# Performance work log

Measured on AMD Instinct MI355X. Metric: run time of the kernel, lower is better.

Reference implementation:

```python
import jax, jax.numpy as jnp
import numpy as np
from jax import lax

B, T, F, H, NSTEPS = 512, 512, 64, 128, 8
HALF = H // 2
LN_EPS = 1e-5


def gru_cell(x, h, w_ih, w_hh, b_ih, b_hh):
    # PyTorch GRUCell math. x: (B, in), h: (B, H)
    gx = x @ w_ih.T + b_ih            # (B, 3H)
    gh = h @ w_hh.T + b_hh            # (B, 3H)
    rx, zx, nx = jnp.split(gx, 3, axis=-1)
    rh, zh, nh = jnp.split(gh, 3, axis=-1)
    r = jax.nn.sigmoid(rx + rh)
    z = jax.nn.sigmoid(zx + zh)
    n = jnp.tanh(nx + r * nh)
    return (1.0 - z) * n + z * h


def run_gru_layer(xs, h0, w_ih, w_hh, b_ih, b_hh):
    # xs: (T, B, in) -> (T, B, H), last hidden (B, H)
    def step(h, x_t):
        h = gru_cell(x_t, h, w_ih, w_hh, b_ih, b_hh)
        return h, h
    h_last, ys = lax.scan(step, h0, xs)
    return ys, h_last


def setup_inputs() -> dict:
    key = jax.random.key(0)
    ks = iter(jax.random.split(key, 64))
    s = 1.0 / np.sqrt(H)

    def p(shape):
        return jax.random.uniform(next(ks), shape, jnp.float32, -s, s)

    inp = {"x": jax.random.normal(next(ks), (B, T, F), jnp.float32)}
    # encoder: 3 GRU layers (layer 0 takes F features, layers 1-2 take H)
    for l, d_in in enumerate([F, H, H]):
        inp[f"e{l}w_ih"] = p((3 * H, d_in))
        inp[f"e{l}w_hh"] = p((3 * H, H))
        inp[f"e{l}b_ih"] = p((3 * H,))
        inp[f"e{l}b_hh"] = p((3 * H,))
    # additive (Bahdanau) attention
    inp["aWq"] = p((H, H)); inp["abq"] = p((H,))
    inp["aWk"] = p((H, H)); inp["abk"] = p((H,))
    inp["av"] = p((H,))
    # decoder GRU: input is cat([context, state]) -> 2H
    inp["dw_ih"] = p((3 * H, 2 * H)); inp["dw_hh"] = p((3 * H, H))
    inp["db_ih"] = p((3 * H,)); inp["db_hh"] = p((3 * H,))
    # head: LayerNorm -> Linear(H, H/2) -> ReLU -> Linear(H/2, 1)
    inp["lng"] = jnp.ones((H,), jnp.float32); inp["lnb"] = jnp.zeros((H,), jnp.float32)
    inp["w1"] = p((HALF, H)); inp["b1"] = p((HALF,))
    inp["w2"] = p((1, HALF)); inp["b2"] = p((1,))
    return inp


def reference(x,
              e0w_ih, e0w_hh, e0b_ih, e0b_hh,
              e1w_ih, e1w_hh, e1b_ih, e1b_hh,
              e2w_ih, e2w_hh, e2b_ih, e2b_hh,
              aWq, abq, aWk, abk, av,
              dw_ih, dw_hh, db_ih, db_hh,
              lng, lnb, w1, b1, w2, b2):
    b = x.shape[0]
    xs = jnp.transpose(x, (1, 0, 2))  # (T, B, F)
    h0 = jnp.zeros((b, H), x.dtype)
    # 3-layer encoder GRU (dropout is eval-mode no-op)
    ys, _ = run_gru_layer(xs, h0, e0w_ih, e0w_hh, e0b_ih, e0b_hh)
    ys, _ = run_gru_layer(ys, h0, e1w_ih, e1w_hh, e1b_ih, e1b_hh)
    ys, h_n = run_gru_layer(ys, h0, e2w_ih, e2w_hh, e2b_ih, e2b_hh)
    enc = jnp.transpose(ys, (1, 0, 2))  # (B, T, H)

    keys = enc @ aWk.T + abk  # precompute key projection once: (B, T, H)

    def dec_step(h, _):
        q = h @ aWq.T + abq                                   # (B, H)
        scores = jnp.einsum('bth,h->bt', jnp.tanh(keys + q[:, None, :]), av)
        w = jax.nn.softmax(scores, axis=-1)                   # (B, T)
        ctx = jnp.einsum('bt,bth->bh', w, enc)                # (B, H)
        h_new = gru_cell(jnp.concatenate([ctx, h], axis=-1), h,
                         dw_ih, dw_hh, db_ih, db_hh)
        mu = h_new.mean(-1, keepdims=True)
        var = ((h_new - mu) ** 2).mean(-1, keepdims=True)
        y = (h_new - mu) / jnp.sqrt(var + LN_EPS) * lng + lnb
        y = jax.nn.relu(y @ w1.T + b1)
        pred = y @ w2.T + b2                                  # (B, 1)
        return h_new, pred

    _, preds = lax.scan(dec_step, h_n, None, length=NSTEPS)   # (n_steps, B, 1)
    return jnp.transpose(preds, (1, 0, 2))                    # (B, n_steps, 1)
```

## Files before the change

kernel.cpp:

```cpp
#include <hip/hip_runtime.h>
#include <hip/hip_bf16.h>
#include <cstdint>
#include <cstddef>

#define T_LEN 512
#define B_SZ  512
#define F_IN  64
#define H_DIM 128
#define NSTEP 8

typedef __attribute__((ext_vector_type(8))) short short8;
typedef __attribute__((ext_vector_type(4))) float f32x4;

__device__ __forceinline__ float fsig(float x) { return 1.0f / (1.0f + __expf(-x)); }
__device__ __forceinline__ float ftanh(float x) {
  float e = __expf(-2.0f * fabsf(x));
  float t = (1.0f - e) / (1.0f + e);
  return copysignf(t, x);
}
__device__ __forceinline__ unsigned short bf16hi(float x) {
  __hip_bfloat16 h = __float2bfloat16(x);
  return *(unsigned short*)&h;
}
__device__ __forceinline__ float bf2f(unsigned short u) {
  return __uint_as_float(((unsigned)u) << 16);
}
__device__ __forceinline__ float bflo(unsigned u) { return __uint_as_float(u << 16); }
__device__ __forceinline__ float bfhi(unsigned u) { return __uint_as_float(u & 0xffff0000u); }

template <int CTRL>
__device__ __forceinline__ float dpp_add(float v) {
  int p = __builtin_amdgcn_update_dpp(0, __float_as_int(v), CTRL, 0xF, 0xF, true);
  return v + __int_as_float(p);
}
__device__ __forceinline__ float row_sum16(float v) {
  v = dpp_add<0xB1>(v);
  v = dpp_add<0x4E>(v);
  v = dpp_add<0x124>(v);
  v = dpp_add<0x128>(v);
  return v;
}

__device__ __forceinline__ void split8(const float* p, short8& hi, short8& lo) {
  #pragma unroll
  for (int i = 0; i < 8; ++i) {
    const float v = p[i];
    const unsigned short h = bf16hi(v);
    hi[i] = (short)h;
    lo[i] = (short)bf16hi(v - bf2f(h));
  }
}

__device__ __forceinline__ void split_f4pair(const float4 a, const float4 b,
                                             short8& hi, short8& lo) {
  const float v[8] = {a.x, a.y, a.z, a.w, b.x, b.y, b.z, b.w};
  #pragma unroll
  for (int j = 0; j < 8; ++j) {
    const unsigned short h = bf16hi(v[j]);
    hi[j] = (short)h;
    lo[j] = (short)bf16hi(v[j] - bf2f(h));
  }
}

__global__ __launch_bounds__(256) void prep_split(
    const float* __restrict__ w0, const float* __restrict__ w1,
    const float* __restrict__ w2,
    unsigned short* __restrict__ hi, unsigned short* __restrict__ lo)
{
  const int i = blockIdx.x * 256 + threadIdx.x;
  if (i >= 122880) return;
  float v = (i < 24576) ? w0[i] : ((i < 73728) ? w1[i - 24576] : w2[i - 73728]);
  const unsigned short h = bf16hi(v);
  hi[i] = h;
  lo[i] = bf16hi(v - bf2f(h));
}

template <int IS_L0>
__global__ __launch_bounds__(512, 2) void rec_fused(
    const float* x,
    const unsigned short* Xhi,
    const unsigned short* Xlo,
    const unsigned short* __restrict__ Wih_hi,
    const unsigned short* __restrict__ Wih_lo,
    const float* __restrict__ w_hh, const float* __restrict__ b_ih,
    const float* __restrict__ b_hh,
    unsigned short* Hhi, unsigned short* Hlo)
{
  constexpr int KD   = IS_L0 ? 64 : 128;
  constexpr int NCK  = KD / 32;
  constexpr int WROW = KD * 2;
  constexpr int WGRAN = WROW / 16;
  constexpr int XBUF = IS_L0 ? 4096 : 8192;

  __shared__ unsigned short Wlds[384 * KD];
  __shared__ float gxlds[8 * 2 * 384];
  __shared__ unsigned short hbh[2][2048], hbl[2][2048];
  __shared__ unsigned short hsh[2][256], hsl[2][256];
  __shared__ __align__(16) unsigned char Xraw[2][XBUF];

  const int tid  = threadIdx.x;
  const int wv   = tid >> 6, lane = tid & 63;
  const int quad = lane >> 4, l16 = lane & 15;
  const int b0   = blockIdx.x * 2;
  const int c    = wv * 16 + l16;

  {
    unsigned char* wb = (unsigned char*)Wlds;
    #pragma unroll
    for (int k = 0; k < (384 * WGRAN) / 512; ++k) {
      const int idx = k * 512 + tid;
      const int row = idx / WGRAN;
      const int gg  = idx % WGRAN;
      const uint4 v = *(const uint4*)&Wih_hi[(size_t)row * KD + gg * 8];
      *(uint4*)&wb[row * WROW + ((gg ^ (row & 7)) * 16)] = v;
    }
  }

  short8 Wl_[3][NCK];
  #pragma unroll
  for (int g_ = 0; g_ < 3; ++g_)
    #pragma unroll
    for (int ck = 0; ck < NCK; ++ck)
      Wl_[g_][ck] = *(const short8*)&Wih_lo[(size_t)(g_ * 128 + c) * KD + ck * 32 + quad * 8];

  short8 Bh[3][4], Bl[3][4];
  #pragma unroll
  for (int g_ = 0; g_ < 3; ++g_)
    #pragma unroll
    for (int ck = 0; ck < 4; ++ck)
      split8(&w_hh[(size_t)(g_ * 128 + c) * 128 + ck * 32 + quad * 8],
             Bh[g_][ck], Bl[g_][ck]);

  float bias_r = 0.f, bias_z = 0.f, bihn = 0.f, bhhn = 0.f, h0 = 0.f, h1 = 0.f;
  if (quad == 0) {
    bias_r = b_ih[c] + b_hh[c];
    bias_z = b_ih[c + 128] + b_hh[c + 128];
    bihn = b_ih[c + 256];
    bhhn = b_hh[c + 256];
    hsh[0][c] = 0; hsh[0][128 + c] = 0;
    hsl[0][c] = 0; hsl[0][128 + c] = 0;
  }

  const int t8 = tid & 255;
  const int sr = t8 >> 4;
  const int sg = tid & 15;
  uint4 xr = {0, 0, 0, 0};

  auto load_xr = [&](int tgn) {
    if constexpr (IS_L0) {
      if (tid < 256)
        xr = *(const uint4*)&x[((size_t)(b0 + (sr & 1)) * T_LEN + tgn + (sr >> 1)) * 64 + sg * 4];
    } else {
      const unsigned short* src = (tid < 256) ? Xhi : Xlo;
      xr = *(const uint4*)&src[((size_t)(tgn + (sr >> 1)) * B_SZ + b0 + (sr & 1)) * 128 + sg * 8];
    }
  };
  auto store_xr = [&](int buf) {
    unsigned char* dstb = &Xraw[buf][0];
    const int off = sr * 256 + ((sg ^ (sr & 7)) * 16);
    if constexpr (IS_L0) {
      if (tid < 256) *(uint4*)&dstb[off] = xr;
    } else {
      *(uint4*)&dstb[(tid < 256 ? 0 : 4096) + off] = xr;
    }
  };
  auto flush_h = [&](int buf, int tp) {
    const int ft = t8 >> 5, fr = (t8 >> 4) & 1, fs = t8 & 15;
    const size_t go = ((size_t)(tp + ft) * B_SZ + b0 + fr) * 128 + fs * 8;
    const int lo_ = (ft * 2 + fr) * 128 + fs * 8;
    if (tid < 256) *(uint4*)&Hhi[go] = *(const uint4*)&hbh[buf][lo_];
    else           *(uint4*)&Hlo[go] = *(const uint4*)&hbl[buf][lo_];
  };

  load_xr(0);
  store_xr(0);
  load_xr(8);
  __syncthreads();

  for (int g = 0; g < 64; ++g) {
    if (g > 0) flush_h((g - 1) & 1, g * 8 - 8);

    short8 Xhf[NCK], Xlf[NCK];
    {
      const unsigned char* xbuf = &Xraw[g & 1][0];
      if constexpr (IS_L0) {
        #pragma unroll
        for (int ck = 0; ck < 2; ++ck) {
          const int g0 = ck * 8 + quad * 2;
          const float4 f0 = *(const float4*)&xbuf[l16 * 256 + ((g0 ^ (l16 & 7)) * 16)];
          const float4 f1 = *(const float4*)&xbuf[l16 * 256 + (((g0 + 1) ^ (l16 & 7)) * 16)];
          split_f4pair(f0, f1, Xhf[ck], Xlf[ck]);
        }
      } else {
        #pragma unroll
        for (int ck = 0; ck < 4; ++ck) {
          const int go = ((ck * 4 + quad) ^ (l16 & 7)) * 16;
          Xhf[ck] = *(const short8*)&xbuf[l16 * 256 + go];
          Xlf[ck] = *(const short8*)&xbuf[4096 + l16 * 256 + go];
        }
      }
    }
    {
      f32x4 ax[3][2];
      #pragma unroll
      for (int g_ = 0; g_ < 3; ++g_) {
        ax[g_][0] = (f32x4){0.f, 0.f, 0.f, 0.f};
        ax[g_][1] = (f32x4){0.f, 0.f, 0.f, 0.f};
      }
      const unsigned char* wb = (const unsigned char*)Wlds;
      #pragma unroll
      for (int ck = 0; ck < NCK; ++ck) {
        const int p = (NCK == 4) ? (ck >> 1) : ck;
        #pragma unroll
        for (int g_ = 0; g_ < 3; ++g_) {
          const int n = g_ * 128 + c;
          const short8 wh = *(const short8*)&wb[n * WROW + (((ck * 4 + quad) ^ (n & 7)) * 16)];
          ax[g_][p] = __builtin_amdgcn_mfma_f32_16x16x32_bf16(Xhf[ck], wh, ax[g_][p], 0, 0, 0);
          ax[g_][p] = __builtin_amdgcn_mfma_f32_16x16x32_bf16(Xhf[ck], Wl_[g_][ck], ax[g_][p], 0, 0, 0);
          ax[g_][p] = __builtin_amdgcn_mfma_f32_16x16x32_bf16(Xlf[ck], wh, ax[g_][p], 0, 0, 0);
        }
      }
      #pragma unroll
      for (int g_ = 0; g_ < 3; ++g_)
        #pragma unroll
        for (int reg = 0; reg < 4; ++reg) {
          const int tt_ = quad * 2 + (reg >> 1);
          const int r_  = reg & 1;
          gxlds[(tt_ * 2 + r_) * 384 + g_ * 128 + c] = ax[g_][0][reg] + ax[g_][1][reg];
        }
    }
    __syncthreads();

    #pragma unroll
    for (int tt = 0; tt < 8; ++tt) {
      float gr0 = 0.f, gz0 = 0.f, gn0 = 0.f, gr1 = 0.f, gz1 = 0.f, gn1 = 0.f;
      if (quad == 0) {
        const float* gp = &gxlds[tt * 768 + c];
        gr0 = gp[0];   gz0 = gp[128]; gn0 = gp[256];
        gr1 = gp[384]; gz1 = gp[512]; gn1 = gp[640];
      }

      short8 Ahf[4], Alf[4];
      if (l16 < 2) {
        #pragma unroll
        for (int ck = 0; ck < 4; ++ck) {
          const int ad = l16 * 128 + ck * 32 + quad * 8;
          Ahf[ck] = *(const short8*)&hsh[tt & 1][ad];
          Alf[ck] = *(const short8*)&hsl[tt & 1][ad];
        }
      } else {
        #pragma unroll
        for (int ck = 0; ck < 4; ++ck) {
          Ahf[ck] = (short8){0, 0, 0, 0, 0, 0, 0, 0};
          Alf[ck] = (short8){0, 0, 0, 0, 0, 0, 0, 0};
        }
      }

      f32x4 acc[3][2];
      #pragma unroll
      for (int g_ = 0; g_ < 3; ++g_) {
        acc[g_][0] = (f32x4){0.f, 0.f, 0.f, 0.f};
        acc[g_][1] = (f32x4){0.f, 0.f, 0.f, 0.f};
      }
      #pragma unroll
      for (int ck = 0; ck < 4; ++ck) {
        const int p = ck >> 1;
        #pragma unroll
        for (int g_ = 0; g_ < 3; ++g_) {
          acc[g_][p] = __builtin_amdgcn_mfma_f32_16x16x32_bf16(Ahf[ck], Bh[g_][ck], acc[g_][p], 0, 0, 0);
          acc[g_][p] = __builtin_amdgcn_mfma_f32_16x16x32_bf16(Ahf[ck], Bl[g_][ck], acc[g_][p], 0, 0, 0);
          acc[g_][p] = __builtin_amdgcn_mfma_f32_16x16x32_bf16(Alf[ck], Bh[g_][ck], acc[g_][p], 0, 0, 0);
        }
      }

      if (quad == 0) {
        const float ghr0 = acc[0][0][0] + acc[0][1][0];
        const float ghr1 = acc[0][0][1] + acc[0][1][1];
        const float ghz0 = acc[1][0][0] + acc[1][1][0];
        const float ghz1 = acc[1][0][1] + acc[1][1][1];
        const float ghn0 = acc[2][0][0] + acc[2][1][0];
        const float ghn1 = acc[2][0][1] + acc[2][1][1];
        const float r0 = fsig(gr0 + ghr0 + bias_r);
        const float z0 = fsig(gz0 + ghz0 + bias_z);
        const float nv0 = ftanh(gn0 + bihn + r0 * (ghn0 + bhhn));
        const float hn0 = (1.0f - z0) * nv0 + z0 * h0;
        const float r1 = fsig(gr1 + ghr1 + bias_r);
        const float z1 = fsig(gz1 + ghz1 + bias_z);
        const float nv1 = ftanh(gn1 + bihn + r1 * (ghn1 + bhhn));
        const float hn1 = (1.0f - z1) * nv1 + z1 * h1;
        h0 = hn0; h1 = hn1;
        const int nb = (tt + 1) & 1;
        const unsigned short hh0 = bf16hi(hn0), hh1 = bf16hi(hn1);
        const unsigned short hl0 = bf16hi(hn0 - bf2f(hh0));
        const unsigned short hl1 = bf16hi(hn1 - bf2f(hh1));
        hsh[nb][c] = hh0;       hsh[nb][128 + c] = hh1;
        hsl[nb][c] = hl0;       hsl[nb][128 + c] = hl1;
        const int hb = (tt * 2) * 128 + c;
        hbh[g & 1][hb] = hh0;       hbh[g & 1][hb + 128] = hh1;
        hbl[g & 1][hb] = hl0;       hbl[g & 1][hb + 128] = hl1;
      }

      if (tt == 7 && g + 1 < 64) {
        store_xr((g + 1) & 1);
        if (g + 2 < 64) load_xr((g + 2) * 8);
      }
      __syncthreads();
    }
  }
  flush_h(1, 504);
}

__global__ __launch_bounds__(256) void keys_gemm(
    const unsigned short* __restrict__ Ahi, const unsigned short* __restrict__ Alo,
    const float* __restrict__ aWk, const float* __restrict__ abk,
    unsigned short* __restrict__ Khi)
{
  __shared__ unsigned short Ah[64 * 40], Al[64 * 40];
  __shared__ unsigned short Bh[128 * 136], Bl[128 * 136];
  const int tid  = threadIdx.x;
  const int wave = tid >> 6, lane = tid & 63;
  const int quad = lane >> 4, l16 = lane & 15;
  const size_t m0 = (size_t)blockIdx.x * 64;

  for (int i = tid; i < 16384; i += 256) {
    const float v = aWk[i];
    const unsigned short h = bf16hi(v);
    const int r = i >> 7, k = i & 127;
    Bh[r * 136 + k] = h;
    Bl[r * 136 + k] = bf16hi(v - bf2f(h));
  }

  f32x4 acc[8];
  #pragma unroll
  for (int i = 0; i < 8; ++i) acc[i] = (f32x4){0.f, 0.f, 0.f, 0.f};
  float bias[8];
  #pragma unroll
  for (int nt = 0; nt < 8; ++nt) bias[nt] = abk[nt * 16 + l16];

  const int r = tid >> 2, c8 = (tid & 3) * 8;
  for (int kc = 0; kc < 128; kc += 32) {
    __syncthreads();
    const size_t src = (m0 + r) * 128 + kc + c8;
    *(uint4*)&Ah[r * 40 + c8] = *(const uint4*)&Ahi[src];
    *(uint4*)&Al[r * 40 + c8] = *(const uint4*)&Alo[src];
    __syncthreads();
    const short8 a_hi = *(const short8*)&Ah[(wave * 16 + l16) * 40 + quad * 8];
    const short8 a_lo = *(const short8*)&Al[(wave * 16 + l16) * 40 + quad * 8];
    #pragma unroll
    for (int nt = 0; nt < 8; ++nt) {
      const short8 b_hi = *(const short8*)&Bh[(nt * 16 + l16) * 136 + kc + quad * 8];
      const short8 b_lo = *(const short8*)&Bl[(nt * 16 + l16) * 136 + kc + quad * 8];
      acc[nt] = __builtin_amdgcn_mfma_f32_16x16x32_bf16(a_hi, b_hi, acc[nt], 0, 0, 0);
      acc[nt] = __builtin_amdgcn_mfma_f32_16x16x32_bf16(a_hi, b_lo, acc[nt], 0, 0, 0);
      acc[nt] = __builtin_amdgcn_mfma_f32_16x16x32_bf16(a_lo, b_hi, acc[nt], 0, 0, 0);
    }
  }
  #pragma unroll
  for (int nt = 0; nt < 8; ++nt) {
    #pragma unroll
    for (int reg = 0; reg < 4; ++reg) {
      const size_t m = m0 + wave * 16 + quad * 4 + reg;
      const int n = nt * 16 + l16;
      Khi[m * 128 + n] = bf16hi(acc[nt][reg] + bias[nt]);
    }
  }
}

__global__ __launch_bounds__(512) void decoder(
    const unsigned short* __restrict__ Hhi, const unsigned short* __restrict__ Hlo,
    const unsigned short* __restrict__ Khi,
    const float* __restrict__ aWq, const float* __restrict__ abq,
    const float* __restrict__ av,
    const float* __restrict__ dwih, const float* __restrict__ dwhh,
    const float* __restrict__ dbih, const float* __restrict__ dbhh,
    const float* __restrict__ lng, const float* __restrict__ lnb,
    const float* __restrict__ w1, const float* __restrict__ b1,
    const float* __restrict__ w2, const float* __restrict__ b2,
    float* __restrict__ out)
{
  __shared__ float h_s[128], q_s[128], av_s[128], s_s[512], w_s[512];
  __shared__ float part[8][128], u_s[256], gx_s[384], gh_s[384], y_s[128];
  __shared__ float red[16];
  const int b = blockIdx.x, tid = threadIdx.x;
  const int wave = tid >> 6, lane = tid & 63;
  const int tslot = lane >> 4, ks = lane & 15;

  if (tid < 128) {
    const size_t base = ((size_t)(T_LEN - 1) * B_SZ + b) * 128 + tid;
    h_s[tid] = bf2f(Hhi[base]) + bf2f(Hlo[base]);
    av_s[tid] = av[tid];
  }
  __syncthreads();

  for (int step = 0; step < NSTEP; ++step) {
    if (tid < 128) {
      float acc = abq[tid];
      const float* wr = &aWq[(size_t)tid * 128];
      #pragma unroll 8
      for (int k4 = 0; k4 < 32; ++k4) {
        const float4 hv = *(const float4*)&h_s[k4 * 4];
        const float4 wv = *(const float4*)&wr[k4 * 4];
        acc += hv.x * wv.x + hv.y * wv.y + hv.z * wv.z + hv.w * wv.w;
      }
      q_s[tid] = acc;
    }
    __syncthreads();
    #pragma unroll 2
    for (int it = 0; it < 16; ++it) {
      const int t = it * 32 + wave * 4 + tslot;
      const size_t kb = ((size_t)t * B_SZ + b) * 128 + ks * 8;
      const uint4 uh = *(const uint4*)&Khi[kb];
      const float4 q0 = *(const float4*)&q_s[ks * 8];
      const float4 q1 = *(const float4*)&q_s[ks * 8 + 4];
      const float4 a0 = *(const float4*)&av_s[ks * 8];
      const float4 a1 = *(const float4*)&av_s[ks * 8 + 4];
      float acc = ftanh(bflo(uh.x) + q0.x) * a0.x + ftanh(bfhi(uh.x) + q0.y) * a0.y
                + ftanh(bflo(uh.y) + q0.z) * a0.z + ftanh(bfhi(uh.y) + q0.w) * a0.w
                + ftanh(bflo(uh.z) + q1.x) * a1.x + ftanh(bfhi(uh.z) + q1.y) * a1.y
                + ftanh(bflo(uh.w) + q1.z) * a1.z + ftanh(bfhi(uh.w) + q1.w) * a1.w;
      acc = row_sum16(acc);
      if (ks == 0) s_s[t] = acc;
    }
    __syncthreads();
    {
      const float sv = s_s[tid];
      float mx = sv;
      #pragma unroll
      for (int o = 32; o; o >>= 1) mx = fmaxf(mx, __shfl_xor(mx, o, 64));
      if (lane == 0) red[wave] = mx;
      __syncthreads();
      mx = red[0];
      #pragma unroll
      for (int i = 1; i < 8; ++i) mx = fmaxf(mx, red[i]);
      const float e = __expf(sv - mx);
      float sm = e;
      #pragma unroll
      for (int o = 32; o; o >>= 1) sm += __shfl_xor(sm, o, 64);
      if (lane == 0) red[8 + wave] = sm;
      __syncthreads();
      float tot = red[8];
      #pragma unroll
      for (int i = 1; i < 8; ++i) tot += red[8 + i];
      w_s[tid] = e / tot;
    }
    __syncthreads();
    {
      const int th = tid >> 6;
      const int c2 = (tid & 63) * 2;
      float acc0 = 0.0f, acc1 = 0.0f;
      #pragma unroll 4
      for (int q = 0; q < 64; ++q) {
        const int t = th * 64 + q;
        const unsigned u = *(const unsigned*)&Hhi[((size_t)t * B_SZ + b) * 128 + c2];
        const float wt = w_s[t];
        acc0 += wt * bflo(u);
        acc1 += wt * bfhi(u);
      }
      part[th][c2] = acc0;
      part[th][c2 + 1] = acc1;
    }
    __syncthreads();
    if (tid < 128) {
      float s = part[0][tid];
      #pragma unroll
      for (int i = 1; i < 8; ++i) s += part[i][tid];
      u_s[tid] = s;
      u_s[128 + tid] = h_s[tid];
    }
    __syncthreads();
    if (tid < 384) {
      const int j = tid;
      float gxv = dbih[j], ghv = dbhh[j];
      const float* wxr = &dwih[(size_t)j * 256];
      const float* whr = &dwhh[(size_t)j * 128];
      #pragma unroll 8
      for (int k4 = 0; k4 < 64; ++k4) {
        const float4 uv = *(const float4*)&u_s[k4 * 4];
        const float4 wv = *(const float4*)&wxr[k4 * 4];
        gxv += uv.x * wv.x + uv.y * wv.y + uv.z * wv.z + uv.w * wv.w;
      }
      #pragma unroll 8
      for (int k4 = 0; k4 < 32; ++k4) {
        const float4 hv = *(const float4*)&h_s[k4 * 4];
        const float4 wv = *(const float4*)&whr[k4 * 4];
        ghv += hv.x * wv.x + hv.y * wv.y + hv.z * wv.z + hv.w * wv.w;
      }
      gx_s[j] = gxv; gh_s[j] = ghv;
    }
    __syncthreads();
    if (tid < 128) {
      const float r = fsig(gx_s[tid] + gh_s[tid]);
      const float z = fsig(gx_s[128 + tid] + gh_s[128 + tid]);
      const float n = ftanh(gx_s[256 + tid] + r * gh_s[256 + tid]);
      const float hn = (1.0f - z) * n + z * h_s[tid];
      h_s[tid] = hn;
      float s1 = hn, s2 = hn * hn;
      #pragma unroll
      for (int o = 32; o; o >>= 1) { s1 += __shfl_xor(s1, o, 64); s2 += __shfl_xor(s2, o, 64); }
      if ((tid & 63) == 0) { red[tid >> 6] = s1; red[4 + (tid >> 6)] = s2; }
    }
    __syncthreads();
    if (tid < 128) {
      const float hn  = h_s[tid];
      const float mu  = (red[0] + red[1]) * (1.0f / 128.0f);
      const float var = (red[4] + red[5]) * (1.0f / 128.0f) - mu * mu;
      y_s[tid] = (hn - mu) / sqrtf(var + 1e-5f) * lng[tid] + lnb[tid];
    }
    __syncthreads();
    if (tid < 64) {
      float acc = b1[tid];
      const float* wr = &w1[(size_t)tid * 128];
      #pragma unroll 8
      for (int k4 = 0; k4 < 32; ++k4) {
        const float4 yv = *(const float4*)&y_s[k4 * 4];
        const float4 wv = *(const float4*)&wr[k4 * 4];
        acc += yv.x * wv.x + yv.y * wv.y + yv.z * wv.z + yv.w * wv.w;
      }
      acc = fmaxf(acc, 0.0f);
      float v = acc * w2[tid];
      #pragma unroll
      for (int o = 32; o; o >>= 1) v += __shfl_xor(v, o, 64);
      if (tid == 0) out[(size_t)b * NSTEP + step] = v + b2[0];
    }
    __syncthreads();
  }
}

extern "C" void kernel_launch(void* const* d_in, const int* in_sizes, int n_in,
                              void* d_out, int out_size, void* d_ws, size_t ws_size,
                              hipStream_t stream)
{
  (void)in_sizes; (void)n_in; (void)out_size; (void)ws_size;
  const float* x    = (const float*)d_in[0];
  const float* ewih[3] = {(const float*)d_in[1], (const float*)d_in[5], (const float*)d_in[9]};
  const float* ewhh[3] = {(const float*)d_in[2], (const float*)d_in[6], (const float*)d_in[10]};
  const float* ebih[3] = {(const float*)d_in[3], (const float*)d_in[7], (const float*)d_in[11]};
  const float* ebhh[3] = {(const float*)d_in[4], (const float*)d_in[8], (const float*)d_in[12]};
  const float* aWq  = (const float*)d_in[13];
  const float* abq  = (const float*)d_in[14];
  const float* aWk  = (const float*)d_in[15];
  const float* abk  = (const float*)d_in[16];
  const float* av   = (const float*)d_in[17];
  const float* dwih = (const float*)d_in[18];
  const float* dwhh = (const float*)d_in[19];
  const float* dbih = (const float*)d_in[20];
  const float* dbhh = (const float*)d_in[21];
  const float* lng  = (const float*)d_in[22];
  const float* lnb  = (const float*)d_in[23];
  const float* w1   = (const float*)d_in[24];
  const float* b1   = (const float*)d_in[25];
  const float* w2   = (const float*)d_in[26];
  const float* b2   = (const float*)d_in[27];

  const size_t HN = (size_t)T_LEN * B_SZ * H_DIM;
  unsigned short* Hhi = (unsigned short*)d_ws;
  unsigned short* Hlo = Hhi + HN;
  float* regionC = (float*)(Hlo + HN);
  unsigned short* Whi = (unsigned short*)(regionC + 25165824 + 65536);
  unsigned short* Wlo = Whi + 122880;
  unsigned short* Khi = (unsigned short*)regionC;

  prep_split<<<dim3(480), dim3(256), 0, stream>>>(ewih[0], ewih[1], ewih[2], Whi, Wlo);

  rec_fused<1><<<dim3(256), dim3(512), 0, stream>>>(
      x, nullptr, nullptr, Whi, Wlo,
      ewhh[0], ebih[0], ebhh[0], Hhi, Hlo);
  rec_fused<0><<<dim3(256), dim3(512), 0, stream>>>(
      nullptr, Hhi, Hlo, Whi + 24576, Wlo + 24576,
      ewhh[1], ebih[1], ebhh[1], Hhi, Hlo);
  rec_fused<0><<<dim3(256), dim3(512), 0, stream>>>(
      nullptr, Hhi, Hlo, Whi + 73728, Wlo + 73728,
      ewhh[2], ebih[2], ebhh[2], Hhi, Hlo);

  keys_gemm<<<dim3(4096), dim3(256), 0, stream>>>(Hhi, Hlo, aWk, abk, Khi);
  decoder<<<dim3(512), dim3(512), 0, stream>>>(
      Hhi, Hlo, Khi, aWq, abq, av, dwih, dwhh, dbih, dbhh,
      lng, lnb, w1, b1, w2, b2, (float*)d_out);
}
```

Before: 2.691 ms.

## Transpose encoder outputs to batch-major for decoder; lighten recurrent step barriers

Keys are written batch-major and a new kernel transposes the encoder hidden states into a batch-major buffer (reusing the Hlo region), so each decoder block reads a contiguous per-batch slab instead of strided rows. The last hidden state is saved to its own buffer before Hlo is overwritten. Inside the recurrent kernel, __syncthreads is replaced by an LDS-only wait plus s_barrier, and the h-fragment loads no longer branch on lane (all lanes load and the MFMA chain starts from zero). The extra transpose kernel adds a full pass over the hidden states, and non-zero A rows could feed garbage into unused output rows.

```diff
diff --git a/kernel.cpp b/kernel.cpp
--- a/kernel.cpp
+++ b/kernel.cpp
@@ -27,6 +27,12 @@
 }
 __device__ __forceinline__ float bflo(unsigned u) { return __uint_as_float(u << 16); }
 __device__ __forceinline__ float bfhi(unsigned u) { return __uint_as_float(u & 0xffff0000u); }
+
+__device__ __forceinline__ void step_barrier() {
+  asm volatile("s_waitcnt lgkmcnt(0)" ::: "memory");
+  __builtin_amdgcn_s_barrier();
+  asm volatile("" ::: "memory");
+}
 
 template <int CTRL>
 __device__ __forceinline__ float dpp_add(float v) {
@@ -103,6 +109,8 @@
   const int quad = lane >> 4, l16 = lane & 15;
   const int b0   = blockIdx.x * 2;
   const int c    = wv * 16 + l16;
+
+  const f32x4 z4 = (f32x4){0.f, 0.f, 0.f, 0.f};
 
   {
     unsigned char* wb = (unsigned char*)Wlds;
@@ -202,12 +210,12 @@
     }
     {
       f32x4 ax[3][2];
+      const unsigned char* wb = (const unsigned char*)Wlds;
       #pragma unroll
       for (int g_ = 0; g_ < 3; ++g_) {
-        ax[g_][0] = (f32x4){0.f, 0.f, 0.f, 0.f};
-        ax[g_][1] = (f32x4){0.f, 0.f, 0.f, 0.f};
-      }
-      const unsigned char* wb = (const unsigned char*)Wlds;
+        ax[g_][0] = z4;
+        ax[g_][1] = z4;
+      }
       #pragma unroll
       for (int ck = 0; ck < NCK; ++ck) {
         const int p = (NCK == 4) ? (ck >> 1) : ck;
@@ -229,47 +237,37 @@
           gxlds[(tt_ * 2 + r_) * 384 + g_ * 128 + c] = ax[g_][0][reg] + ax[g_][1][reg];
         }
     }
-    __syncthreads();
+    step_barrier();
 
     #pragma unroll
     for (int tt = 0; tt < 8; ++tt) {
-      float gr0 = 0.f, gz0 = 0.f, gn0 = 0.f, gr1 = 0.f, gz1 = 0.f, gn1 = 0.f;
+      float gr0 = 0.f, gz0 = 0.f, gn0v = 0.f, gr1 = 0.f, gz1 = 0.f, gn1v = 0.f;
       if (quad == 0) {
         const float* gp = &gxlds[tt * 768 + c];
-        gr0 = gp[0];   gz0 = gp[128]; gn0 = gp[256];
-        gr1 = gp[384]; gz1 = gp[512]; gn1 = gp[640];
+        gr0 = gp[0];   gz0 = gp[128]; gn0v = gp[256];
+        gr1 = gp[384]; gz1 = gp[512]; gn1v = gp[640];
       }
 
       short8 Ahf[4], Alf[4];
-      if (l16 < 2) {
+      #pragma unroll
+      for (int ck = 0; ck < 4; ++ck) {
+        const int ad = (l16 & 1) * 128 + ck * 32 + quad * 8;
+        Ahf[ck] = *(const short8*)&hsh[tt & 1][ad];
+        Alf[ck] = *(const short8*)&hsl[tt & 1][ad];
+      }
+
+      f32x4 acc[3][2];
+      #pragma unroll
+      for (int g_ = 0; g_ < 3; ++g_) {
         #pragma unroll
-        for (int ck = 0; ck < 4; ++ck) {
-          const int ad = l16 * 128 + ck * 32 + quad * 8;
-          Ahf[ck] = *(const short8*)&hsh[tt & 1][ad];
-          Alf[ck] = *(const short8*)&hsl[tt & 1][ad];
-        }
-      } else {
-        #pragma unroll
-        for (int ck = 0; ck < 4; ++ck) {
-          Ahf[ck] = (short8){0, 0, 0, 0, 0, 0, 0, 0};
-          Alf[ck] = (short8){0, 0, 0, 0, 0, 0, 0, 0};
-        }
-      }
-
-      f32x4 acc[3][2];
-      #pragma unroll
-      for (int g_ = 0; g_ < 3; ++g_) {
-        acc[g_][0] = (f32x4){0.f, 0.f, 0.f, 0.f};
-        acc[g_][1] = (f32x4){0.f, 0.f, 0.f, 0.f};
-      }
-      #pragma unroll
-      for (int ck = 0; ck < 4; ++ck) {
-        const int p = ck >> 1;
-        #pragma unroll
-        for (int g_ = 0; g_ < 3; ++g_) {
-          acc[g_][p] = __builtin_amdgcn_mfma_f32_16x16x32_bf16(Ahf[ck], Bh[g_][ck], acc[g_][p], 0, 0, 0);
-          acc[g_][p] = __builtin_amdgcn_mfma_f32_16x16x32_bf16(Ahf[ck], Bl[g_][ck], acc[g_][p], 0, 0, 0);
-          acc[g_][p] = __builtin_amdgcn_mfma_f32_16x16x32_bf16(Alf[ck], Bh[g_][ck], acc[g_][p], 0, 0, 0);
+        for (int p = 0; p < 2; ++p) {
+          const int k0 = p * 2;
+          acc[g_][p] = __builtin_amdgcn_mfma_f32_16x16x32_bf16(Ahf[k0], Bh[g_][k0], z4, 0, 0, 0);
+          acc[g_][p] = __builtin_amdgcn_mfma_f32_16x16x32_bf16(Ahf[k0], Bl[g_][k0], acc[g_][p], 0, 0, 0);
+          acc[g_][p] = __builtin_amdgcn_mfma_f32_16x16x32_bf16(Alf[k0], Bh[g_][k0], acc[g_][p], 0, 0, 0);
+          acc[g_][p] = __builtin_amdgcn_mfma_f32_16x16x32_bf16(Ahf[k0 + 1], Bh[g_][k0 + 1], acc[g_][p], 0, 0, 0);
+          acc[g_][p] = __builtin_amdgcn_mfma_f32_16x16x32_bf16(Ahf[k0 + 1], Bl[g_][k0 + 1], acc[g_][p], 0, 0, 0);
+          acc[g_][p] = __builtin_amdgcn_mfma_f32_16x16x32_bf16(Alf[k0 + 1], Bh[g_][k0 + 1], acc[g_][p], 0, 0, 0);
         }
       }
 
@@ -282,11 +280,11 @@
         const float ghn1 = acc[2][0][1] + acc[2][1][1];
         const float r0 = fsig(gr0 + ghr0 + bias_r);
         const float z0 = fsig(gz0 + ghz0 + bias_z);
-        const float nv0 = ftanh(gn0 + bihn + r0 * (ghn0 + bhhn));
+        const float nv0 = ftanh(gn0v + bihn + r0 * (ghn0 + bhhn));
         const float hn0 = (1.0f - z0) * nv0 + z0 * h0;
         const float r1 = fsig(gr1 + ghr1 + bias_r);
         const float z1 = fsig(gz1 + ghz1 + bias_z);
-        const float nv1 = ftanh(gn1 + bihn + r1 * (ghn1 + bhhn));
+        const float nv1 = ftanh(gn1v + bihn + r1 * (ghn1 + bhhn));
         const float hn1 = (1.0f - z1) * nv1 + z1 * h1;
         h0 = hn0; h1 = hn1;
         const int nb = (tt + 1) & 1;
@@ -304,7 +302,7 @@
         store_xr((g + 1) & 1);
         if (g + 2 < 64) load_xr((g + 2) * 8);
       }
-      __syncthreads();
+      step_barrier();
     }
   }
   flush_h(1, 504);
@@ -313,7 +311,7 @@
 __global__ __launch_bounds__(256) void keys_gemm(
     const unsigned short* __restrict__ Ahi, const unsigned short* __restrict__ Alo,
     const float* __restrict__ aWk, const float* __restrict__ abk,
-    unsigned short* __restrict__ Khi)
+    unsigned short* __restrict__ Kbt)
 {
   __shared__ unsigned short Ah[64 * 40], Al[64 * 40];
   __shared__ unsigned short Bh[128 * 136], Bl[128 * 136];
@@ -360,15 +358,42 @@
     #pragma unroll
     for (int reg = 0; reg < 4; ++reg) {
       const size_t m = m0 + wave * 16 + quad * 4 + reg;
+      const size_t b = m & 511, t = m >> 9;
       const int n = nt * 16 + l16;
-      Khi[m * 128 + n] = bf16hi(acc[nt][reg] + bias[nt]);
-    }
+      Kbt[(b * T_LEN + t) * 128 + n] = bf16hi(acc[nt][reg] + bias[nt]);
+    }
+  }
+}
+
+__global__ __launch_bounds__(512) void save_lasth(
+    const unsigned short* __restrict__ Hhi, const unsigned short* __restrict__ Hlo,
+    float* __restrict__ lastH)
+{
+  const int i = blockIdx.x * 512 + threadIdx.x;
+  const size_t src = ((size_t)(T_LEN - 1) * B_SZ) * 128 + i;
+  lastH[i] = bf2f(Hhi[src]) + bf2f(Hlo[src]);
+}
+
+__global__ __launch_bounds__(256) void transpose_h(
+    const unsigned short* __restrict__ Hhi, unsigned short* __restrict__ Hbt)
+{
+  const int b  = blockIdx.x >> 3;
+  const int tg = blockIdx.x & 7;
+  #pragma unroll
+  for (int j = 0; j < 4; ++j) {
+    const int id = threadIdx.x * 4 + j;
+    const int tl = id >> 4;
+    const int ch = (id & 15) * 8;
+    const int t  = tg * 64 + tl;
+    const uint4 v = *(const uint4*)&Hhi[((size_t)t * B_SZ + b) * 128 + ch];
+    *(uint4*)&Hbt[((size_t)b * T_LEN + t) * 128 + ch] = v;
   }
 }
 
 __global__ __launch_bounds__(512) void decoder(
-    const unsigned short* __restrict__ Hhi, const unsigned short* __restrict__ Hlo,
-    const unsigned short* __restrict__ Khi,
+    const unsigned short* __restrict__ Hbt,
+    const unsigned short* __restrict__ Kbt,
+    const float* __restrict__ lastH,
     const float* __restrict__ aWq, const float* __restrict__ abq,
     const float* __restrict__ av,
     const float* __restrict__ dwih, const float* __restrict__ dwhh,
@@ -386,8 +411,7 @@
   const int tslot = lane >> 4, ks = lane & 15;
 
   if (tid < 128) {
-    const size_t base = ((size_t)(T_LEN - 1) * B_SZ + b) * 128 + tid;
-    h_s[tid] = bf2f(Hhi[base]) + bf2f(Hlo[base]);
+    h_s[tid] = lastH[(size_t)b * 128 + tid];
     av_s[tid] = av[tid];
   }
   __syncthreads();
@@ -408,8 +432,8 @@
     #pragma unroll 2
     for (int it = 0; it < 16; ++it) {
       const int t = it * 32 + wave * 4 + tslot;
-      const size_t kb = ((size_t)t * B_SZ + b) * 128 + ks * 8;
-      const uint4 uh = *(const uint4*)&Khi[kb];
+      const size_t kb = ((size_t)b * T_LEN + t) * 128 + ks * 8;
+      const uint4 uh = *(const uint4*)&Kbt[kb];
       const float4 q0 = *(const float4*)&q_s[ks * 8];
       const float4 q1 = *(const float4*)&q_s[ks * 8 + 4];
       const float4 a0 = *(const float4*)&av_s[ks * 8];
@@ -451,7 +475,7 @@
       #pragma unroll 4
       for (int q = 0; q < 64; ++q) {
         const int t = th * 64 + q;
-        const unsigned u = *(const unsigned*)&Hhi[((size_t)t * B_SZ + b) * 128 + c2];
+        const unsigned u = *(const unsigned*)&Hbt[((size_t)b * T_LEN + t) * 128 + c2];
         const float wt = w_s[t];
         acc0 += wt * bflo(u);
         acc1 += wt * bfhi(u);
@@ -558,7 +582,8 @@
   float* regionC = (float*)(Hlo + HN);
   unsigned short* Whi = (unsigned short*)(regionC + 25165824 + 65536);
   unsigned short* Wlo = Whi + 122880;
-  unsigned short* Khi = (unsigned short*)regionC;
+  unsigned short* Kbt = (unsigned short*)regionC;
+  float* lastH = regionC + 16777216;
 
   prep_split<<<dim3(480), dim3(256), 0, stream>>>(ewih[0], ewih[1], ewih[2], Whi, Wlo);
 
@@ -572,8 +597,10 @@
       nullptr, Hhi, Hlo, Whi + 73728, Wlo + 73728,
       ewhh[2], ebih[2], ebhh[2], Hhi, Hlo);
 
-  keys_gemm<<<dim3(4096), dim3(256), 0, stream>>>(Hhi, Hlo, aWk, abk, Khi);
+  keys_gemm<<<dim3(4096), dim3(256), 0, stream>>>(Hhi, Hlo, aWk, abk, Kbt);
+  save_lasth<<<dim3(128), dim3(512), 0, stream>>>(Hhi, Hlo, lastH);
+  transpose_h<<<dim3(4096), dim3(256), 0, stream>>>(Hhi, Hlo);
   decoder<<<dim3(512), dim3(512), 0, stream>>>(
-      Hhi, Hlo, Khi, aWq, abq, av, dwih, dwhh, dbih, dbhh,
+      Hlo, Kbt, lastH, aWq, abq, av, dwih, dwhh, dbih, dbhh,
       lng, lnb, w1, b1, w2, b2, (float*)d_out);
 }
```

Result: faster. 2.630 ms (-2.3%).
